# Kernel optimization log

Hardware: AMD Instinct MI355X
Metric: run time of the kernel (lower is better)

Reference implementation:

```python
import jax, jax.numpy as jnp
import numpy as np

COMMIT_WEIGHT = 0.25  # cfg.commit_weight


def setup_inputs() -> dict:
    key = jax.random.key(0)
    k1, k2 = jax.random.split(key)
    z = jax.random.normal(k1, (262144, 64), dtype=jnp.float32)
    codebook = jax.random.normal(k2, (512, 64), dtype=jnp.float32) * 0.02
    return {"z": z, "codebook": codebook}


def reference(z, codebook):
    # projector = Identity (apply_sim_vq=False)
    # squared euclidean distances [N, K]; argmin matches cdist(p=2) argmin
    d2 = (
        jnp.sum(z * z, axis=-1, keepdims=True)
        - 2.0 * (z @ codebook.T)
        + jnp.sum(codebook * codebook, axis=-1)
    )
    ids = jnp.argmin(d2, axis=-1)          # [N] int
    q = codebook[ids]                       # [N, D] gather
    loss = (
        jnp.mean((jax.lax.stop_gradient(z) - q) ** 2)
        + COMMIT_WEIGHT * jnp.mean((jax.lax.stop_gradient(q) - z) ** 2)
    )
    # straight-through estimator (training path)
    q_ste = z + jax.lax.stop_gradient(q - z)
    return q_ste, loss, ids
```

## Files before the change

kernel.cpp:

```cpp
#include <hip/hip_runtime.h>
#include <math.h>


constexpr int D     = 64;
constexpr int D4    = 16;
constexpr int K     = 512;
constexpr float STH = 2e-4f;

typedef __attribute__((ext_vector_type(8)))  short s16x8;
typedef __attribute__((ext_vector_type(16))) float f32x16;

#define FMA4(acc, zz, cc) do { \
  acc = fmaf((zz).x, (cc).x, acc); \
  acc = fmaf((zz).y, (cc).y, acc); \
  acc = fmaf((zz).z, (cc).z, acc); \
  acc = fmaf((zz).w, (cc).w, acc); } while (0)

__device__ __forceinline__ unsigned short f2bf(float f) {
  unsigned u = __float_as_uint(f);
  return (unsigned short)((u + 0x7FFFu + ((u >> 16) & 1u)) >> 16);
}

__global__ void vq_prep(const float* __restrict__ cbk,
                        float* __restrict__ nhc2arr,
                        float* __restrict__ c2s,
                        unsigned short* __restrict__ cbh,
                        unsigned short* __restrict__ cbl)
{
  int cw = blockIdx.x * 64 + threadIdx.x;
  if (cw >= K) return;
  const float4* c4 = (const float4*)(cbk + (size_t)cw * D);
  float s = 0.f;
  #pragma unroll
  for (int i = 0; i < D4; ++i) {
    float4 f = c4[i];
    FMA4(s, f, f);
    float e[4] = {f.x, f.y, f.z, f.w};
    unsigned short hh[4], ll[4];
    #pragma unroll
    for (int j = 0; j < 4; ++j) {
      unsigned short hb = f2bf(e[j]);
      float hf = __uint_as_float((unsigned)hb << 16);
      hh[j] = hb; ll[j] = f2bf(e[j] - hf);
    }
    ushort4 hv, lv;
    hv.x = hh[0]; hv.y = hh[1]; hv.z = hh[2]; hv.w = hh[3];
    lv.x = ll[0]; lv.y = ll[1]; lv.z = ll[2]; lv.w = ll[3];
    *(ushort4*)(cbh + (size_t)cw * D + i * 4) = hv;
    *(ushort4*)(cbl + (size_t)cw * D + i * 4) = lv;
  }
  c2s[cw] = s;
  int t = cw >> 5, w = cw & 31;
  int ai = (t << 5) + (((w >> 2) & 1) << 4) + ((w >> 3) << 2) + (w & 3);
  nhc2arr[ai] = -0.5f * s;
}


#define MFMA_B(A, B, C) __builtin_amdgcn_mfma_f32_32x32x16_bf16(A, B, C, 0, 0, 0)

#define LDS_FRAGS(CH, CL, T) do { \
  int b0_ = (((T) * 32 + col) << 7) + (h << 4); \
  CH[0] = *(const s16x8*)(smem + ((b0_      ) ^ xsw)); \
  CH[1] = *(const s16x8*)(smem + ((b0_ + 32 ) ^ xsw)); \
  CH[2] = *(const s16x8*)(smem + ((b0_ + 64 ) ^ xsw)); \
  CH[3] = *(const s16x8*)(smem + ((b0_ + 96 ) ^ xsw)); \
  CL[0] = *(const s16x8*)(smem + ((b0_ + 65536      ) ^ xsw)); \
  CL[1] = *(const s16x8*)(smem + ((b0_ + 65536 + 32 ) ^ xsw)); \
  CL[2] = *(const s16x8*)(smem + ((b0_ + 65536 + 64 ) ^ xsw)); \
  CL[3] = *(const s16x8*)(smem + ((b0_ + 65536 + 96 ) ^ xsw)); \
} while (0)

#define LDS_GG(G, T) do { \
  int gb_ = 131072 + ((((T) << 5) + (h << 4)) << 2); \
  G[0] = *(const float4*)(smem + gb_); \
  G[1] = *(const float4*)(smem + gb_ + 16); \
  G[2] = *(const float4*)(smem + gb_ + 32); \
  G[3] = *(const float4*)(smem + gb_ + 48); \
} while (0)

#define TILE_BODY(T, CH, CL, G) do { \
  f32x16 acc0 = {}, acc1 = {}; \
  acc0 = MFMA_B(CH[0], zh[0], acc0);  acc1 = MFMA_B(CH[1], zh[1], acc1); \
  acc0 = MFMA_B(CH[2], zh[2], acc0);  acc1 = MFMA_B(CH[3], zh[3], acc1); \
  acc0 = MFMA_B(CH[0], zl[0], acc0);  acc1 = MFMA_B(CH[1], zl[1], acc1); \
  acc0 = MFMA_B(CH[2], zl[2], acc0);  acc1 = MFMA_B(CH[3], zl[3], acc1); \
  acc0 = MFMA_B(CL[0], zh[0], acc0);  acc1 = MFMA_B(CL[1], zh[1], acc1); \
  acc0 = MFMA_B(CL[2], zh[2], acc0);  acc1 = MFMA_B(CL[3], zh[3], acc1); \
  const float ggv[16] = {G[0].x, G[0].y, G[0].z, G[0].w, \
                         G[1].x, G[1].y, G[1].z, G[1].w, \
                         G[2].x, G[2].y, G[2].z, G[2].w, \
                         G[3].x, G[3].y, G[3].z, G[3].w}; \
  float m1a = -INFINITY, m2a = -INFINITY, m1b = -INFINITY, m2b = -INFINITY; \
  int ra_ = 0, rb_ = 8; \
  _Pragma("unroll") \
  for (int r = 0; r < 8; ++r) { \
    float v = (acc0[r] + acc1[r]) + ggv[r]; \
    bool gt = v > m1a; \
    m2a = fminf(fmaxf(v, m2a), m1a); \
    if (gt) ra_ = r; \
    m1a = gt ? v : m1a; \
  } \
  _Pragma("unroll") \
  for (int r = 8; r < 16; ++r) { \
    float v = (acc0[r] + acc1[r]) + ggv[r]; \
    bool gt = v > m1b; \
    m2b = fminf(fmaxf(v, m2b), m1b); \
    if (gt) rb_ = r; \
    m1b = gt ? v : m1b; \
  } \
   \
  float tm1 = fmaxf(m1a, m1b); \
  float tm2 = fmaxf(fminf(m1a, m1b), fmaxf(m2a, m2b)); \
  int   tr_ = (m1b > m1a) ? rb_ : ra_;    \
  bool tgt = tm1 > m1;                    \
  m2 = fmaxf(fminf(tm1, m1), fmaxf(tm2, m2)); \
  if (tgt) { rbest = tr_; tbest = (T); } \
  m1 = tgt ? tm1 : m1; \
} while (0)

__global__ __launch_bounds__(512)
void vq_mfma(const float* __restrict__ z, const float* __restrict__ cbk,
             float* __restrict__ out, float* __restrict__ lossAcc,
             const unsigned short* __restrict__ cbh,
             const float* __restrict__ nhc2arr,
             unsigned* __restrict__ cnt, unsigned* __restrict__ list, int N)
{
  extern __shared__ char smem[];

  const int tid  = threadIdx.x;
  const int lane = tid & 63;
  const int wave = tid >> 6;
  const int col  = lane & 31;
  const int h    = lane >> 5;
  const int xsw  = (col & 7) << 4;

  {
    const char* gt = (const char*)cbh;
    #pragma unroll 4
    for (int i = tid; i < 8192; i += 512) {
      int gb = i << 4;
      int sb = gb ^ (((gb >> 7) & 7) << 4);
      *(float4*)(smem + sb) = *(const float4*)(gt + gb);
    }
    if (tid < 128)
      *(float4*)(smem + 131072 + (tid << 4)) = ((const float4*)nhc2arr)[tid];
  }
  __syncthreads();

  float lacc = 0.f;

  #pragma unroll 1
  for (int it = 0; it < 4; ++it) {
    const long rowg = (long)blockIdx.x * 1024 + it * 256 + wave * 32 + col;

    const float4* zp4 = (const float4*)(z + (size_t)rowg * D);
    s16x8 zh[4], zl[4];
    #pragma unroll
    for (int s = 0; s < 4; ++s) {
      float4 p0 = zp4[4 * s + 2 * h];
      float4 p1 = zp4[4 * s + 2 * h + 1];
      float e[8] = {p0.x, p0.y, p0.z, p0.w, p1.x, p1.y, p1.z, p1.w};
      #pragma unroll
      for (int j = 0; j < 8; ++j) {
        unsigned short hb = f2bf(e[j]);
        float hf = __uint_as_float((unsigned)hb << 16);
        zh[s][j] = (short)hb;
        zl[s][j] = (short)f2bf(e[j] - hf);
      }
    }

    float m1 = -INFINITY, m2 = -INFINITY;
    int rbest = 0, tbest = 0;

    s16x8 chA[4], clA[4], chB[4], clB[4];
    float4 gA[4], gB[4];
    LDS_FRAGS(chA, clA, 0);  LDS_GG(gA, 0);
    LDS_FRAGS(chB, clB, 1);  LDS_GG(gB, 1);
    #pragma unroll 1
    for (int t = 0; t < 14; t += 2) {
      TILE_BODY(t, chA, clA, gA);
      LDS_FRAGS(chA, clA, t + 2);  LDS_GG(gA, t + 2);
      TILE_BODY(t + 1, chB, clB, gB);
      LDS_FRAGS(chB, clB, t + 3);  LDS_GG(gB, t + 3);
    }
    TILE_BODY(14, chA, clA, gA);
    TILE_BODY(15, chB, clB, gB);

    int idx = (tbest << 5) + (h << 2) + (rbest & 3) + ((rbest >> 2) << 3);

    float om1  = __shfl_xor(m1, 32);
    float om2  = __shfl_xor(m2, 32);
    int   oidx = __shfl_xor(idx, 32);
    float nm2 = fmaxf(fminf(m1, om1), fmaxf(m2, om2));
    bool take = (om1 > m1) || ((om1 == m1) && (oidx < idx));
    if (take) { m1 = om1; idx = oidx; }
    m2 = nm2;

    if (m1 - m2 > STH) {
      const float4* qp = (const float4*)(cbk + (size_t)idx * D) + (h << 3);
      const float4* zp = (const float4*)(z + (size_t)rowg * D) + (h << 3);
      float4*       op = (float4*)(out + (size_t)rowg * D) + (h << 3);
      #pragma unroll
      for (int i = 0; i < 8; ++i) {
        float4 q = qp[i], zz = zp[i], u, qs;
        u.x = q.x - zz.x; u.y = q.y - zz.y; u.z = q.z - zz.z; u.w = q.w - zz.w;
        qs.x = zz.x + u.x; qs.y = zz.y + u.y; qs.z = zz.z + u.z; qs.w = zz.w + u.w;
        FMA4(lacc, u, u);
        op[i] = qs;
      }
      if (h == 0) (out + (size_t)N * D + 1)[rowg] = (float)idx;
    } else if (h == 0) {
      unsigned p = atomicAdd(cnt, 1u);
      list[p] = (unsigned)rowg;
    }
  }

  #pragma unroll
  for (int off = 32; off > 0; off >>= 1) lacc += __shfl_down(lacc, off, 64);
  if (lane == 0) atomicAdd(lossAcc, lacc);
}

__global__ __launch_bounds__(256)
void vq_fallback(const float* __restrict__ z, const float* __restrict__ cbk,
                 float* __restrict__ out, float* __restrict__ lossAcc,
                 const float* __restrict__ c2s,
                 const unsigned* __restrict__ list,
                 const unsigned* __restrict__ cntp, int N)
{
  const unsigned cnt = *cntp;
  const int lane = threadIdx.x & 63;
  const unsigned wid = (blockIdx.x * blockDim.x + threadIdx.x) >> 6;
  const unsigned nw  = (gridDim.x * blockDim.x) >> 6;

  float lacc = 0.f;
  #pragma unroll 1
  for (unsigned p = wid; p < cnt; p += nw) {
    const size_t r0 = (size_t)list[p];

    const float4* zp = (const float4*)(z + r0 * D);
    float4 z0[D4];
    #pragma unroll
    for (int i = 0; i < D4; ++i) z0[i] = zp[i];
    float z2 = 0.f;
    #pragma unroll
    for (int i = 0; i < D4; ++i) FMA4(z2, z0[i], z0[i]);

    float best = INFINITY;
    int   bi = 0;
    #pragma unroll 1
    for (int j = 0; j < 8; ++j) {
      const int k = (lane << 3) + j;
      const float4* c4 = (const float4*)(cbk + (size_t)k * D);
      float4 cr[D4];
      #pragma unroll
      for (int i = 0; i < D4; ++i) cr[i] = c4[i];
      float c2 = c2s[k];
      float a0 = 0.f, b0 = 0.f;
      #pragma unroll
      for (int i = 0; i < 8; ++i) {
        FMA4(a0, z0[2 * i],     cr[2 * i]);
        FMA4(b0, z0[2 * i + 1], cr[2 * i + 1]);
      }
      float dot = a0 + b0;
      float d = fmaf(-2.f, dot, z2) + c2;
      if (d < best) { best = d; bi = k; }
    }

    #pragma unroll
    for (int off = 32; off > 0; off >>= 1) {
      float ob = __shfl_xor(best, off, 64);
      int  obi = __shfl_xor(bi, off, 64);
      if (ob < best || (ob == best && obi < bi)) { best = ob; bi = obi; }
    }

    if (lane == 0) {
      const float4* qp = (const float4*)(cbk + (size_t)bi * D);
      float4* o = (float4*)(out + r0 * D);
      #pragma unroll
      for (int i = 0; i < D4; ++i) {
        float4 q = qp[i], zz = z0[i], u, qs;
        u.x = q.x - zz.x; u.y = q.y - zz.y; u.z = q.z - zz.z; u.w = q.w - zz.w;
        qs.x = zz.x + u.x; qs.y = zz.y + u.y; qs.z = zz.z + u.z; qs.w = zz.w + u.w;
        FMA4(lacc, u, u);
        o[i] = qs;
      }
      (out + (size_t)N * D + 1)[r0] = (float)bi;
    }
  }
  if (lacc != 0.f) atomicAdd(lossAcc, lacc);
}

__global__ void vq_finalize(float* __restrict__ out,
                            const float* __restrict__ lossAcc, int N)
{
  out[(size_t)N * D] = 1.25f * (lossAcc[0] / (float)((long)N * D));
}

extern "C" void kernel_launch(void* const* d_in, const int* in_sizes, int n_in,
                              void* d_out, int out_size, void* d_ws, size_t ws_size,
                              hipStream_t stream)
{
  const float* z   = (const float*)d_in[0];
  const float* cbk = (const float*)d_in[1];
  float* out = (float*)d_out;
  float* ws  = (float*)d_ws;
  const int N = in_sizes[0] / D;

  float*          lossAcc = ws;
  unsigned*       cnt     = (unsigned*)(ws + 1);
  float*          nhc2arr = ws + 64;
  float*          c2s     = ws + 576;
  unsigned short* cbh     = (unsigned short*)(ws + 1536);
  unsigned short* cbl     = cbh + K * D;
  unsigned*       list    = (unsigned*)(ws + 34304);

  hipMemsetAsync(ws, 0, 8, stream);
  vq_prep<<<8, 64, 0, stream>>>(cbk, nhc2arr, c2s, cbh, cbl);
  vq_mfma<<<N / 1024, 512, 133120, stream>>>(z, cbk, out, lossAcc, cbh,
                                             nhc2arr, cnt, list, N);
  vq_fallback<<<1024, 256, 0, stream>>>(z, cbk, out, lossAcc, c2s, list, cnt, N);
  vq_finalize<<<1, 1, 0, stream>>>(out, lossAcc, N);
}
```

Baseline: 214.6 us.

## Fuse codebook prep, fallback and finalize into single VQ kernel

Removes the separate prep, fallback and finalize kernels. Each block now converts the codebook to hi/lo bf16 fragments directly in LDS using a new unswizzled, fragment-ordered layout. Ambiguous rows are rescanned inline by the same wave instead of being appended to a global list, and the last block to finish writes the loss. The bias term now seeds the MFMA accumulator rather than being added afterward. This saves launch overhead and global round-trips, but every block redoes the codebook conversion, the unswizzled layout may cause LDS bank conflicts, and inline fallback can stall waves.

After: 225.7 us. 1.05x slower.

```diff
diff --git a/kernel.cpp b/kernel.cpp
--- a/kernel.cpp
+++ b/kernel.cpp
@@ -16,62 +16,28 @@
   acc = fmaf((zz).z, (cc).z, acc); \
   acc = fmaf((zz).w, (cc).w, acc); } while (0)
 
+#define MFMA_B(A, B, C) __builtin_amdgcn_mfma_f32_32x32x16_bf16(A, B, C, 0, 0, 0)
+
 __device__ __forceinline__ unsigned short f2bf(float f) {
   unsigned u = __float_as_uint(f);
   return (unsigned short)((u + 0x7FFFu + ((u >> 16) & 1u)) >> 16);
 }
 
-__global__ void vq_prep(const float* __restrict__ cbk,
-                        float* __restrict__ nhc2arr,
-                        float* __restrict__ c2s,
-                        unsigned short* __restrict__ cbh,
-                        unsigned short* __restrict__ cbl)
-{
-  int cw = blockIdx.x * 64 + threadIdx.x;
-  if (cw >= K) return;
-  const float4* c4 = (const float4*)(cbk + (size_t)cw * D);
-  float s = 0.f;
-  #pragma unroll
-  for (int i = 0; i < D4; ++i) {
-    float4 f = c4[i];
-    FMA4(s, f, f);
-    float e[4] = {f.x, f.y, f.z, f.w};
-    unsigned short hh[4], ll[4];
-    #pragma unroll
-    for (int j = 0; j < 4; ++j) {
-      unsigned short hb = f2bf(e[j]);
-      float hf = __uint_as_float((unsigned)hb << 16);
-      hh[j] = hb; ll[j] = f2bf(e[j] - hf);
-    }
-    ushort4 hv, lv;
-    hv.x = hh[0]; hv.y = hh[1]; hv.z = hh[2]; hv.w = hh[3];
-    lv.x = ll[0]; lv.y = ll[1]; lv.z = ll[2]; lv.w = ll[3];
-    *(ushort4*)(cbh + (size_t)cw * D + i * 4) = hv;
-    *(ushort4*)(cbl + (size_t)cw * D + i * 4) = lv;
-  }
-  c2s[cw] = s;
-  int t = cw >> 5, w = cw & 31;
-  int ai = (t << 5) + (((w >> 2) & 1) << 4) + ((w >> 3) << 2) + (w & 3);
-  nhc2arr[ai] = -0.5f * s;
-}
-
-
-#define MFMA_B(A, B, C) __builtin_amdgcn_mfma_f32_32x32x16_bf16(A, B, C, 0, 0, 0)
 
 #define LDS_FRAGS(CH, CL, T) do { \
-  int b0_ = (((T) * 32 + col) << 7) + (h << 4); \
-  CH[0] = *(const s16x8*)(smem + ((b0_      ) ^ xsw)); \
-  CH[1] = *(const s16x8*)(smem + ((b0_ + 32 ) ^ xsw)); \
-  CH[2] = *(const s16x8*)(smem + ((b0_ + 64 ) ^ xsw)); \
-  CH[3] = *(const s16x8*)(smem + ((b0_ + 96 ) ^ xsw)); \
-  CL[0] = *(const s16x8*)(smem + ((b0_ + 65536      ) ^ xsw)); \
-  CL[1] = *(const s16x8*)(smem + ((b0_ + 65536 + 32 ) ^ xsw)); \
-  CL[2] = *(const s16x8*)(smem + ((b0_ + 65536 + 64 ) ^ xsw)); \
-  CL[3] = *(const s16x8*)(smem + ((b0_ + 65536 + 96 ) ^ xsw)); \
+  const int fb_ = (T) * 4096 + h * 512 + col * 16; \
+  CH[0] = *(const s16x8*)(smem + fb_); \
+  CH[1] = *(const s16x8*)(smem + fb_ + 1024); \
+  CH[2] = *(const s16x8*)(smem + fb_ + 2048); \
+  CH[3] = *(const s16x8*)(smem + fb_ + 3072); \
+  CL[0] = *(const s16x8*)(smem + 65536 + fb_); \
+  CL[1] = *(const s16x8*)(smem + 65536 + fb_ + 1024); \
+  CL[2] = *(const s16x8*)(smem + 65536 + fb_ + 2048); \
+  CL[3] = *(const s16x8*)(smem + 65536 + fb_ + 3072); \
 } while (0)
 
 #define LDS_GG(G, T) do { \
-  int gb_ = 131072 + ((((T) << 5) + (h << 4)) << 2); \
+  const int gb_ = 131072 + (((T) * 32 + h * 16) << 2); \
   G[0] = *(const float4*)(smem + gb_); \
   G[1] = *(const float4*)(smem + gb_ + 16); \
   G[2] = *(const float4*)(smem + gb_ + 32); \
@@ -79,30 +45,31 @@
 } while (0)
 
 #define TILE_BODY(T, CH, CL, G) do { \
-  f32x16 acc0 = {}, acc1 = {}; \
+  f32x16 acc0, acc1 = {};             \
+  acc0[0]  = G[0].x; acc0[1]  = G[0].y; acc0[2]  = G[0].z; acc0[3]  = G[0].w; \
+  acc0[4]  = G[1].x; acc0[5]  = G[1].y; acc0[6]  = G[1].z; acc0[7]  = G[1].w; \
+  acc0[8]  = G[2].x; acc0[9]  = G[2].y; acc0[10] = G[2].z; acc0[11] = G[2].w; \
+  acc0[12] = G[3].x; acc0[13] = G[3].y; acc0[14] = G[3].z; acc0[15] = G[3].w; \
   acc0 = MFMA_B(CH[0], zh[0], acc0);  acc1 = MFMA_B(CH[1], zh[1], acc1); \
   acc0 = MFMA_B(CH[2], zh[2], acc0);  acc1 = MFMA_B(CH[3], zh[3], acc1); \
   acc0 = MFMA_B(CH[0], zl[0], acc0);  acc1 = MFMA_B(CH[1], zl[1], acc1); \
   acc0 = MFMA_B(CH[2], zl[2], acc0);  acc1 = MFMA_B(CH[3], zl[3], acc1); \
   acc0 = MFMA_B(CL[0], zh[0], acc0);  acc1 = MFMA_B(CL[1], zh[1], acc1); \
   acc0 = MFMA_B(CL[2], zh[2], acc0);  acc1 = MFMA_B(CL[3], zh[3], acc1); \
-  const float ggv[16] = {G[0].x, G[0].y, G[0].z, G[0].w, \
-                         G[1].x, G[1].y, G[1].z, G[1].w, \
-                         G[2].x, G[2].y, G[2].z, G[2].w, \
-                         G[3].x, G[3].y, G[3].z, G[3].w}; \
+   \
   float m1a = -INFINITY, m2a = -INFINITY, m1b = -INFINITY, m2b = -INFINITY; \
   int ra_ = 0, rb_ = 8; \
   _Pragma("unroll") \
   for (int r = 0; r < 8; ++r) { \
-    float v = (acc0[r] + acc1[r]) + ggv[r]; \
-    bool gt = v > m1a; \
-    m2a = fminf(fmaxf(v, m2a), m1a); \
+    float v = acc0[r] + acc1[r];        \
+    bool gt = v > m1a;                  \
+    m2a = fminf(fmaxf(v, m2a), m1a);    \
     if (gt) ra_ = r; \
     m1a = gt ? v : m1a; \
   } \
   _Pragma("unroll") \
   for (int r = 8; r < 16; ++r) { \
-    float v = (acc0[r] + acc1[r]) + ggv[r]; \
+    float v = acc0[r] + acc1[r]; \
     bool gt = v > m1b; \
     m2b = fminf(fmaxf(v, m2b), m1b); \
     if (gt) rb_ = r; \
@@ -118,12 +85,10 @@
   m1 = tgt ? tm1 : m1; \
 } while (0)
 
-__global__ __launch_bounds__(512)
-void vq_mfma(const float* __restrict__ z, const float* __restrict__ cbk,
+__global__ __launch_bounds__(512, 2)
+void vq_main(const float* __restrict__ z, const float* __restrict__ cbk,
              float* __restrict__ out, float* __restrict__ lossAcc,
-             const unsigned short* __restrict__ cbh,
-             const float* __restrict__ nhc2arr,
-             unsigned* __restrict__ cnt, unsigned* __restrict__ list, int N)
+             unsigned* __restrict__ done, int N)
 {
   extern __shared__ char smem[];
 
@@ -132,18 +97,42 @@
   const int wave = tid >> 6;
   const int col  = lane & 31;
   const int h    = lane >> 5;
-  const int xsw  = (col & 7) << 4;
 
   {
-    const char* gt = (const char*)cbh;
-    #pragma unroll 4
-    for (int i = tid; i < 8192; i += 512) {
-      int gb = i << 4;
-      int sb = gb ^ (((gb >> 7) & 7) << 4);
-      *(float4*)(smem + sb) = *(const float4*)(gt + gb);
-    }
-    if (tid < 128)
-      *(float4*)(smem + 131072 + (tid << 4)) = ((const float4*)nhc2arr)[tid];
+    const int cw = tid;
+    const float4* c4 = (const float4*)(cbk + (size_t)cw * D);
+    float4 f[16];
+    #pragma unroll
+    for (int i = 0; i < D4; ++i) f[i] = c4[i];
+    float c2 = 0.f;
+    #pragma unroll
+    for (int i = 0; i < D4; ++i) FMA4(c2, f[i], f[i]);
+    float e[64];
+    #pragma unroll
+    for (int i = 0; i < D4; ++i) {
+      e[4*i] = f[i].x; e[4*i+1] = f[i].y; e[4*i+2] = f[i].z; e[4*i+3] = f[i].w;
+    }
+    const int T = cw >> 5, cc = cw & 31;
+    #pragma unroll
+    for (int sl = 0; sl < 4; ++sl) {
+      #pragma unroll
+      for (int h2 = 0; h2 < 2; ++h2) {
+        const int ld0 = sl * 16 + h2 * 8;
+        s16x8 vh, vl;
+        #pragma unroll
+        for (int j = 0; j < 8; ++j) {
+          unsigned short hb = f2bf(e[ld0 + j]);
+          float hf = __uint_as_float((unsigned)hb << 16);
+          vh[j] = (short)hb;
+          vl[j] = (short)f2bf(e[ld0 + j] - hf);
+        }
+        const int a = T * 4096 + sl * 1024 + h2 * 512 + cc * 16;
+        *(s16x8*)(smem + a) = vh;
+        *(s16x8*)(smem + 65536 + a) = vl;
+      }
+    }
+    const int ai = (T << 5) + (((cc >> 2) & 1) << 4) + ((cc >> 3) << 2) + (cc & 3);
+    *(float*)(smem + 131072 + ai * 4) = -0.5f * c2;
   }
   __syncthreads();
 
@@ -196,7 +185,8 @@
     if (take) { m1 = om1; idx = oidx; }
     m2 = nm2;
 
-    if (m1 - m2 > STH) {
+    const bool certain = (m1 - m2 > STH);
+    if (certain) {
       const float4* qp = (const float4*)(cbk + (size_t)idx * D) + (h << 3);
       const float4* zp = (const float4*)(z + (size_t)rowg * D) + (h << 3);
       float4*       op = (float4*)(out + (size_t)rowg * D) + (h << 3);
@@ -209,91 +199,79 @@
         op[i] = qs;
       }
       if (h == 0) (out + (size_t)N * D + 1)[rowg] = (float)idx;
-    } else if (h == 0) {
-      unsigned p = atomicAdd(cnt, 1u);
-      list[p] = (unsigned)rowg;
+    }
+
+    unsigned mask32 = (unsigned)__ballot((!certain) && h == 0);
+    while (mask32) {
+      const int c = __builtin_ctz(mask32);
+      mask32 &= mask32 - 1;
+      const size_t r0 = (size_t)blockIdx.x * 1024 + it * 256 + wave * 32 + c;
+      const float4* zp = (const float4*)(z + r0 * D);
+      float4 z0[D4];
+      #pragma unroll
+      for (int i = 0; i < D4; ++i) z0[i] = zp[i];
+      float z2 = 0.f;
+      #pragma unroll
+      for (int i = 0; i < D4; ++i) FMA4(z2, z0[i], z0[i]);
+
+      float best = INFINITY;
+      int   bi = 0;
+      #pragma unroll 1
+      for (int j = 0; j < 8; ++j) {
+        const int k = (lane << 3) + j;
+        const float4* c4 = (const float4*)(cbk + (size_t)k * D);
+        float4 cr[D4];
+        #pragma unroll
+        for (int i = 0; i < D4; ++i) cr[i] = c4[i];
+        float c2 = 0.f;
+        #pragma unroll
+        for (int i = 0; i < D4; ++i) FMA4(c2, cr[i], cr[i]);
+        float a0 = 0.f, b0 = 0.f;
+        #pragma unroll
+        for (int i = 0; i < 8; ++i) {
+          FMA4(a0, z0[2 * i],     cr[2 * i]);
+          FMA4(b0, z0[2 * i + 1], cr[2 * i + 1]);
+        }
+        float dot = a0 + b0;
+        float d = fmaf(-2.f, dot, z2) + c2;
+        if (d < best) { best = d; bi = k; }
+      }
+
+      #pragma unroll
+      for (int off = 32; off > 0; off >>= 1) {
+        float ob = __shfl_xor(best, off, 64);
+        int  obi = __shfl_xor(bi, off, 64);
+        if (ob < best || (ob == best && obi < bi)) { best = ob; bi = obi; }
+      }
+
+      if (lane == 0) {
+        const float4* qp = (const float4*)(cbk + (size_t)bi * D);
+        float4* o = (float4*)(out + r0 * D);
+        #pragma unroll
+        for (int i = 0; i < D4; ++i) {
+          float4 q = qp[i], zz = z0[i], u, qs;
+          u.x = q.x - zz.x; u.y = q.y - zz.y; u.z = q.z - zz.z; u.w = q.w - zz.w;
+          qs.x = zz.x + u.x; qs.y = zz.y + u.y; qs.z = zz.z + u.z; qs.w = zz.w + u.w;
+          FMA4(lacc, u, u);
+          o[i] = qs;
+        }
+        (out + (size_t)N * D + 1)[r0] = (float)bi;
+      }
     }
   }
 
   #pragma unroll
   for (int off = 32; off > 0; off >>= 1) lacc += __shfl_down(lacc, off, 64);
   if (lane == 0) atomicAdd(lossAcc, lacc);
-}
-
-__global__ __launch_bounds__(256)
-void vq_fallback(const float* __restrict__ z, const float* __restrict__ cbk,
-                 float* __restrict__ out, float* __restrict__ lossAcc,
-                 const float* __restrict__ c2s,
-                 const unsigned* __restrict__ list,
-                 const unsigned* __restrict__ cntp, int N)
-{
-  const unsigned cnt = *cntp;
-  const int lane = threadIdx.x & 63;
-  const unsigned wid = (blockIdx.x * blockDim.x + threadIdx.x) >> 6;
-  const unsigned nw  = (gridDim.x * blockDim.x) >> 6;
-
-  float lacc = 0.f;
-  #pragma unroll 1
-  for (unsigned p = wid; p < cnt; p += nw) {
-    const size_t r0 = (size_t)list[p];
-
-    const float4* zp = (const float4*)(z + r0 * D);
-    float4 z0[D4];
-    #pragma unroll
-    for (int i = 0; i < D4; ++i) z0[i] = zp[i];
-    float z2 = 0.f;
-    #pragma unroll
-    for (int i = 0; i < D4; ++i) FMA4(z2, z0[i], z0[i]);
-
-    float best = INFINITY;
-    int   bi = 0;
-    #pragma unroll 1
-    for (int j = 0; j < 8; ++j) {
-      const int k = (lane << 3) + j;
-      const float4* c4 = (const float4*)(cbk + (size_t)k * D);
-      float4 cr[D4];
-      #pragma unroll
-      for (int i = 0; i < D4; ++i) cr[i] = c4[i];
-      float c2 = c2s[k];
-      float a0 = 0.f, b0 = 0.f;
-      #pragma unroll
-      for (int i = 0; i < 8; ++i) {
-        FMA4(a0, z0[2 * i],     cr[2 * i]);
-        FMA4(b0, z0[2 * i + 1], cr[2 * i + 1]);
-      }
-      float dot = a0 + b0;
-      float d = fmaf(-2.f, dot, z2) + c2;
-      if (d < best) { best = d; bi = k; }
-    }
-
-    #pragma unroll
-    for (int off = 32; off > 0; off >>= 1) {
-      float ob = __shfl_xor(best, off, 64);
-      int  obi = __shfl_xor(bi, off, 64);
-      if (ob < best || (ob == best && obi < bi)) { best = ob; bi = obi; }
-    }
-
-    if (lane == 0) {
-      const float4* qp = (const float4*)(cbk + (size_t)bi * D);
-      float4* o = (float4*)(out + r0 * D);
-      #pragma unroll
-      for (int i = 0; i < D4; ++i) {
-        float4 q = qp[i], zz = z0[i], u, qs;
-        u.x = q.x - zz.x; u.y = q.y - zz.y; u.z = q.z - zz.z; u.w = q.w - zz.w;
-        qs.x = zz.x + u.x; qs.y = zz.y + u.y; qs.z = zz.z + u.z; qs.w = zz.w + u.w;
-        FMA4(lacc, u, u);
-        o[i] = qs;
-      }
-      (out + (size_t)N * D + 1)[r0] = (float)bi;
+  __syncthreads();
+  if (tid == 0) {
+    __threadfence();
+    unsigned d = atomicAdd(done, 1u);
+    if (d == gridDim.x - 1) {
+      float total = atomicAdd(lossAcc, 0.0f);
+      out[(size_t)N * D] = 1.25f * (total / (float)((long)N * D));
     }
   }
-  if (lacc != 0.f) atomicAdd(lossAcc, lacc);
-}
-
-__global__ void vq_finalize(float* __restrict__ out,
-                            const float* __restrict__ lossAcc, int N)
-{
-  out[(size_t)N * D] = 1.25f * (lossAcc[0] / (float)((long)N * D));
 }
 
 extern "C" void kernel_launch(void* const* d_in, const int* in_sizes, int n_in,
@@ -306,18 +284,9 @@
   float* ws  = (float*)d_ws;
   const int N = in_sizes[0] / D;
 
-  float*          lossAcc = ws;
-  unsigned*       cnt     = (unsigned*)(ws + 1);
-  float*          nhc2arr = ws + 64;
-  float*          c2s     = ws + 576;
-  unsigned short* cbh     = (unsigned short*)(ws + 1536);
-  unsigned short* cbl     = cbh + K * D;
-  unsigned*       list    = (unsigned*)(ws + 34304);
+  float*    lossAcc = ws;
+  unsigned* done    = (unsigned*)(ws + 1);
 
   hipMemsetAsync(ws, 0, 8, stream);
-  vq_prep<<<8, 64, 0, stream>>>(cbk, nhc2arr, c2s, cbh, cbl);
-  vq_mfma<<<N / 1024, 512, 133120, stream>>>(z, cbk, out, lossAcc, cbh,
-                                             nhc2arr, cnt, list, N);
-  vq_fallback<<<1024, 256, 0, stream>>>(z, cbk, out, lossAcc, c2s, list, cnt, N);
-  vq_finalize<<<1, 1, 0, stream>>>(out, lossAcc, N);
+  vq_main<<<N / 1024, 512, 133120, stream>>>(z, cbk, out, lossAcc, done, N);
 }
```
